# Performance work log

Measured on AMD Instinct MI355X. Metric: run time of the kernel, lower is better.

Reference implementation:

```python
import jax, jax.numpy as jnp
import numpy as np

B = 32768
STATE, BELIEF, HID, EMB, ACT = 100, 200, 200, 1024, 32
MIN_STD = 0.1

def _dense_init(key, fan_in, fan_out):
    k1, k2 = jax.random.split(key)
    scale = 1.0 / np.sqrt(fan_in)
    W = jax.random.uniform(k1, (fan_in, fan_out), jnp.float32, -scale, scale)
    b = jnp.zeros((fan_out,), jnp.float32)
    return W, b

def setup_inputs() -> dict:
    key = jax.random.key(0)
    ks = jax.random.split(key, 20)
    inp = {
        'prev_state': jax.random.normal(ks[0], (1, B, STATE), jnp.float32),
        'prev_action': jax.random.normal(ks[1], (1, B, ACT), jnp.float32),
        'prev_belief': jax.random.normal(ks[2], (1, B, BELIEF), jnp.float32),
        'observation': jax.random.normal(ks[3], (1, B, EMB), jnp.float32),
        'nonterminals': jnp.ones((1, B, 1), jnp.float32),
    }
    # fc_embed_state_action: (state+action) -> belief_dim, relu
    inp['W_sa'], inp['b_sa'] = _dense_init(ks[4], STATE + ACT, BELIEF)
    # GRUCell: carry = hidden (belief_dim), inputs = prev_belief (belief_dim)
    inp['W_ir'], inp['b_ir'] = _dense_init(ks[5], BELIEF, BELIEF)
    inp['W_iz'], inp['b_iz'] = _dense_init(ks[6], BELIEF, BELIEF)
    inp['W_in'], inp['b_in'] = _dense_init(ks[7], BELIEF, BELIEF)
    inp['W_hr'], _ = _dense_init(ks[8], BELIEF, BELIEF)   # no bias (flax GRUCell)
    inp['W_hz'], _ = _dense_init(ks[9], BELIEF, BELIEF)   # no bias
    inp['W_hn'], inp['b_hn'] = _dense_init(ks[10], BELIEF, BELIEF)
    # prior head
    inp['W_bp'], inp['b_bp'] = _dense_init(ks[11], BELIEF, HID)
    inp['W_sp'], inp['b_sp'] = _dense_init(ks[12], HID, 2 * STATE)
    # posterior head
    inp['W_bq'], inp['b_bq'] = _dense_init(ks[13], BELIEF + EMB, HID)
    inp['W_sq'], inp['b_sq'] = _dense_init(ks[14], HID, 2 * STATE)
    return inp

def reference(prev_state, prev_action, prev_belief, observation, nonterminals,
              W_sa, b_sa, W_ir, b_ir, W_iz, b_iz, W_in, b_in,
              W_hr, W_hz, W_hn, b_hn,
              W_bp, b_bp, W_sp, b_sp, W_bq, b_bq, W_sq, b_sq):
    noise_key = jax.random.key(42)  # stands in for the module's fixed self.rng
    s = prev_state * nonterminals  # broadcast mask over last dim
    # fc_embed_state_action (relu, activate_final=True)
    h = jax.nn.relu(jnp.concatenate([s, prev_action], axis=-1) @ W_sa + b_sa)
    # flax GRUCell with carry = h, inputs = prev_belief
    x = prev_belief
    r = jax.nn.sigmoid(x @ W_ir + b_ir + h @ W_hr)
    z = jax.nn.sigmoid(x @ W_iz + b_iz + h @ W_hz)
    n = jnp.tanh(x @ W_in + b_in + r * (h @ W_hn + b_hn))
    new_belief = (1.0 - z) * n + z * h
    # prior
    hp = jax.nn.relu(new_belief @ W_bp + b_bp)
    prior_out = jax.nn.relu(hp @ W_sp + b_sp)  # activate_final=True
    prior_mean, prior_std_raw = jnp.split(prior_out, 2, axis=-1)
    prior_std = jax.nn.softplus(prior_std_raw) + MIN_STD
    eps = jax.random.normal(noise_key, prior_mean.shape, prior_mean.dtype)
    prior_state = prior_mean + prior_std * eps
    # posterior
    hq = jax.nn.relu(jnp.concatenate([new_belief, observation], axis=-1) @ W_bq + b_bq)
    post_out = jax.nn.relu(hq @ W_sq + b_sq)
    post_mean, post_std_raw = jnp.split(post_out, 2, axis=-1)
    post_std = jax.nn.softplus(post_std_raw) + MIN_STD
    eps2 = jax.random.normal(noise_key, post_mean.shape, post_mean.dtype)  # same rng reused, as in source
    post_state = post_mean + post_std * eps2
    return (new_belief, prior_state, prior_mean, prior_std, post_state, post_mean, post_std)
```

## Files before the change

### kernel.cpp

```cpp
#include <hip/hip_runtime.h>
#include <stdint.h>

typedef short short8 __attribute__((ext_vector_type(8)));
typedef float floatx4 __attribute__((ext_vector_type(4)));
typedef unsigned short ushort_t;

#define BATCH 32768
#define STR   232
#define SLAB  (16*STR)
#define TOT_TILES 1391

#define M_SA 0
#define M_IR 1
#define M_HR 2
#define M_IZ 3
#define M_HZ 4
#define M_IN 5
#define M_HN 6
#define M_BP 7
#define M_SP 8
#define M_SQ 9
#define M_BQ 10

__device__ constexpr int TILE0[11] = {0,65,156,247,338,429,520,611,702,793,884};
__device__ constexpr int KLIM[11]  = {132,200,200,200,200,200,200,200,200,200,0};

__device__ __forceinline__ ushort_t f2bf(float f){
  uint32_t u = __float_as_uint(f);
  uint32_t r = (u + 0x7fffu + ((u >> 16) & 1u)) >> 16;
  return (ushort_t)r;
}
__device__ __forceinline__ float bf2f(ushort_t h){ return __uint_as_float(((uint32_t)h) << 16); }

__device__ __forceinline__ float sigmf_(float x){ return 1.f / (1.f + expf(-x)); }
__device__ __forceinline__ float softplusf_(float x){
  return fmaxf(x, 0.f) + log1pf(expf(-fabsf(x)));
}
__device__ __forceinline__ uint32_t rotl32(uint32_t x, int r){ return (x << r) | (x >> (32 - r)); }

__device__ __forceinline__ void threefry2x32_k42(uint32_t x0, uint32_t x1,
                                                 uint32_t& o0, uint32_t& o1){
  const uint32_t k0 = 0u, k1 = 42u, k2 = 0u ^ 42u ^ 0x1BD11BDAu;
  x0 += k0; x1 += k1;
#define TF_R(rot) { x0 += x1; x1 = rotl32(x1, rot); x1 ^= x0; }
  TF_R(13) TF_R(15) TF_R(26) TF_R(6)  x0 += k1; x1 += k2 + 1u;
  TF_R(17) TF_R(29) TF_R(16) TF_R(24) x0 += k2; x1 += k0 + 2u;
  TF_R(13) TF_R(15) TF_R(26) TF_R(6)  x0 += k0; x1 += k1 + 3u;
  TF_R(17) TF_R(29) TF_R(16) TF_R(24) x0 += k1; x1 += k2 + 4u;
  TF_R(13) TF_R(15) TF_R(26) TF_R(6)  x0 += k2; x1 += k0 + 5u;
#undef TF_R
  o0 = x0; o1 = x1;
}

__device__ __forceinline__ float jax_erfinv(float x){
  float w = -log1pf(-x * x);
  float p;
  if (w < 5.0f) {
    w -= 2.5f;
    p = 2.81022636e-08f;
    p = fmaf(p, w, 3.43273939e-07f);
    p = fmaf(p, w, -3.5233877e-06f);
    p = fmaf(p, w, -4.39150654e-06f);
    p = fmaf(p, w, 0.00021858087f);
    p = fmaf(p, w, -0.00125372503f);
    p = fmaf(p, w, -0.00417768164f);
    p = fmaf(p, w, 0.246640727f);
    p = fmaf(p, w, 1.50140941f);
  } else {
    w = sqrtf(w) - 3.0f;
    p = -0.000200214257f;
    p = fmaf(p, w, 0.000100950558f);
    p = fmaf(p, w, 0.00134934322f);
    p = fmaf(p, w, -0.00367342844f);
    p = fmaf(p, w, 0.00573950773f);
    p = fmaf(p, w, -0.0076224613f);
    p = fmaf(p, w, 0.00943887047f);
    p = fmaf(p, w, 1.00167406f);
    p = fmaf(p, w, 2.83297682f);
  }
  return p * x;
}

__device__ __forceinline__ float jax_normal_at(uint32_t j){
  uint32_t o0, o1;
  threefry2x32_k42(0u, j, o0, o1);
  uint32_t bits = o0 ^ o1;
  const float lo = -0.99999994f;
  float f = __uint_as_float((bits >> 9) | 0x3f800000u) - 1.0f;
  float fm = f * 1.99999994f;
  float u = fmaxf(lo, fm + lo);
  return 1.41421356f * jax_erfinv(u);
}

struct ConvP { const float* src[11]; ushort_t* dst; };

__global__ void __launch_bounds__(64) convw(ConvP cp)
{
  int t = blockIdx.x;
  int lane = threadIdx.x;
  const int cum[12] = {0,65,156,247,338,429,520,611,702,793,884,1391};
  int mi = 0;
  #pragma unroll
  for (int i = 0; i < 11; ++i) if (t >= cum[i+1]) mi = i+1;
  int lt = t - cum[mi];
  int kb = lt / 13, nt = lt - kb*13;
  const float* S = cp.src[mi];
  int q = lane >> 4, m = lane & 15;
  int n = nt*16 + m;
  ushort_t* D = cp.dst + (size_t)t*512 + lane*8;
  #pragma unroll
  for (int j = 0; j < 8; ++j){
    int k = kb*32 + q*8 + j;
    float v = 0.f;
    if (n < 200){
      if (mi == 10){
        if (k < 200) v = S[k*200+n];
        else if (k >= 224) v = S[(size_t)(k-24)*200+n];
      } else {
        int K = (mi == 0) ? 132 : 200;
        if (k < K) v = S[k*200+n];
      }
    }
    D[j] = f2bf(v);
  }
}

struct MainP {
  const float* prev_state; const float* prev_action; const float* prev_belief;
  const float* observation; const float* nonterm;
  const float* b_sa; const float* b_ir; const float* b_iz; const float* b_in; const float* b_hn;
  const float* b_bp; const float* b_sp; const float* b_bq; const float* b_sq;
  const float* W[11];
  const ushort_t* ws;
  float* out;
};

__device__ __forceinline__ short8 afrag(const ushort_t* buf, int m, int kb, int q){
  return *(const short8*)(buf + m*STR + kb*32 + q*8);
}

#define NSTEPS 214
#define STAGE_US 3584

struct Sched {
  short t0[NSTEPS]; signed char cnt[NSTEPS];
  constexpr Sched() : t0(), cnt() {
    int s = 0;
    for (int kb = 0; kb < 5; ++kb){
      t0[s] = (short)(0 + kb*13);     cnt[s] = 7; ++s;
      t0[s] = (short)(0 + kb*13 + 7); cnt[s] = 6; ++s;
    }
    for (int kb = 0; kb < 7; ++kb)
      for (int mt = 1; mt <= 6; ++mt){ t0[s] = (short)(65 + 91*(mt-1) + kb*13);     cnt[s] = 7; ++s; }
    for (int kb = 0; kb < 7; ++kb)
      for (int mt = 1; mt <= 6; ++mt){ t0[s] = (short)(65 + 91*(mt-1) + kb*13 + 7); cnt[s] = 6; ++s; }
    for (int kb = 0; kb < 7; ++kb){
      t0[s] = (short)(611 + kb*13);     cnt[s] = 7; ++s;
      t0[s] = (short)(611 + kb*13 + 7); cnt[s] = 6; ++s;
    }
    for (int kb = 0; kb < 7; ++kb){
      t0[s] = (short)(702 + kb*13);     cnt[s] = 7; ++s;
      t0[s] = (short)(702 + kb*13 + 7); cnt[s] = 6; ++s;
    }
    for (int kb = 0; kb < 39; ++kb){
      t0[s] = (short)(884 + kb*13);     cnt[s] = 7; ++s;
      t0[s] = (short)(884 + kb*13 + 7); cnt[s] = 6; ++s;
    }
    for (int kb = 0; kb < 7; ++kb){
      t0[s] = (short)(793 + kb*13);     cnt[s] = 7; ++s;
      t0[s] = (short)(793 + kb*13 + 7); cnt[s] = 6; ++s;
    }
  }
};
__device__ constexpr Sched SCHED{};

__device__ __forceinline__ void stage_issue(const ushort_t* ws, ushort_t* sbuf,
                                            int step, int w, int lane)
{
  if (step >= NSTEPS) return;
  const int t0 = SCHED.t0[step];
  const int cn = SCHED.cnt[step];
  ushort_t* dstb = sbuf + (step % 3) * STAGE_US;
  const ushort_t* srcb = ws + ((size_t)t0 << 9) + (lane << 3);
  #pragma unroll
  for (int r = 0; r < 2; ++r){
    int tt = w + r*4;
    if (tt < cn){
      __builtin_amdgcn_global_load_lds(
        (const __attribute__((address_space(1))) uint32_t*)(const void*)(srcb + (tt << 9)),
        (__attribute__((address_space(3)))       uint32_t*)(void*)(dstb + (tt << 9)),
        16, 0, 0);
    }
  }
}

__device__ __forceinline__ short8 sfrag(const ushort_t* sbuf, int step, int j, int lane){
  return *(const short8*)(sbuf + (step % 3) * STAGE_US + (j << 9) + (lane << 3));
}

__device__ __forceinline__ void step_sync(int sidx, int w, int extra)
{
  int n2 = 0;
  if (sidx + 2 < NSTEPS){
    int cn = SCHED.cnt[sidx + 2];
    n2 = (w < cn ? 1 : 0) + ((w + 4) < cn ? 1 : 0);
  }
  int nw = n2 + extra;
  switch (nw){
    case 0:  asm volatile("s_waitcnt vmcnt(0)" ::: "memory"); break;
    case 1:  asm volatile("s_waitcnt vmcnt(1)" ::: "memory"); break;
    case 2:  asm volatile("s_waitcnt vmcnt(2)" ::: "memory"); break;
    case 3:  asm volatile("s_waitcnt vmcnt(3)" ::: "memory"); break;
    default: asm volatile("s_waitcnt vmcnt(4)" ::: "memory"); break;
  }
  __builtin_amdgcn_s_barrier();
}

__device__ __forceinline__ void gemm13_kb(const MainP& p, ushort_t* stageb, int& sidx,
    const ushort_t* asrc, floatx4 (&acc)[13], int kb, int m, int q, int lane, int w)
{
  short8 a = afrag(asrc, m, kb, q);
  stage_issue(p.ws, stageb, sidx+2, w, lane);
  #pragma unroll
  for (int j = 0; j < 7; ++j)
    acc[j] = __builtin_amdgcn_mfma_f32_16x16x32_bf16(a, sfrag(stageb, sidx, j, lane), acc[j], 0,0,0);
  step_sync(sidx, w, 0); ++sidx;
  stage_issue(p.ws, stageb, sidx+2, w, lane);
  #pragma unroll
  for (int j = 0; j < 6; ++j)
    acc[7+j] = __builtin_amdgcn_mfma_f32_16x16x32_bf16(a, sfrag(stageb, sidx, j, lane), acc[7+j], 0,0,0);
  step_sync(sidx, w, 0); ++sidx;
}

template<int CNT, int NT0>
__device__ __forceinline__ void gru_chunk_staged(const MainP& p, ushort_t* stageb, int& sidx,
    const ushort_t* bufX, const ushort_t* bufH, int R0, int m, int q, int lane, int w,
    floatx4 (&nbv)[13])
{
  floatx4 aR[CNT], aZ[CNT], aXN[CNT], aHN[CNT];
  #pragma unroll
  for (int i = 0; i < CNT; ++i){
    int col = (NT0+i)*16 + m;
    float br = (col<200)? p.b_ir[col] : 0.f;
    float bz = (col<200)? p.b_iz[col] : 0.f;
    float bn = (col<200)? p.b_in[col] : 0.f;
    float bh = (col<200)? p.b_hn[col] : 0.f;
    aR[i]  = (floatx4){br,br,br,br};
    aZ[i]  = (floatx4){bz,bz,bz,bz};
    aXN[i] = (floatx4){bn,bn,bn,bn};
    aHN[i] = (floatx4){bh,bh,bh,bh};
  }
#define GRU_STEP(AV, ACC) \
  stage_issue(p.ws, stageb, sidx+2, w, lane); \
  _Pragma("unroll") \
  for (int i = 0; i < CNT; ++i) \
    ACC[i] = __builtin_amdgcn_mfma_f32_16x16x32_bf16(AV, sfrag(stageb, sidx, i, lane), ACC[i], 0,0,0); \
  step_sync(sidx, w, 0); ++sidx;

  #pragma unroll 1
  for (int kb = 0; kb < 7; ++kb){
    short8 ax = afrag(bufX, m, kb, q);
    short8 ah = afrag(bufH, m, kb, q);
    GRU_STEP(ax, aR)
    GRU_STEP(ah, aR)
    GRU_STEP(ax, aZ)
    GRU_STEP(ah, aZ)
    GRU_STEP(ax, aXN)
    GRU_STEP(ah, aHN)
  }
#undef GRU_STEP
  #pragma unroll
  for (int i = 0; i < CNT; ++i){
    int col = (NT0+i)*16 + m;
    if (col < 200){
      #pragma unroll
      for (int rg = 0; rg < 4; ++rg){
        int rowl = q*4 + rg;
        float rr = sigmf_(aR[i][rg]);
        float zz = sigmf_(aZ[i][rg]);
        float nn = tanhf(fmaf(rr, aHN[i][rg], aXN[i][rg]));
        float hv = bf2f(bufH[rowl*STR + col]);
        float nb = fmaf(zz, hv - nn, nn);
        nbv[NT0+i][rg] = nb;
        __builtin_nontemporal_store(nb, &p.out[(size_t)(R0+rowl)*200 + col]);
      }
    }
  }
}

__device__ __forceinline__ void head_out(const floatx4* acc, float* sdb,
    float* o_state, float* o_mean, float* o_std, int R0, int m, int q)
{
  #pragma unroll
  for (int nt = 6; nt < 13; ++nt){
    int col = nt*16 + m;
    if (col >= 100 && col < 200){
      #pragma unroll
      for (int rg = 0; rg < 4; ++rg){
        int rowl = q*4 + rg;
        float sr = fmaxf(acc[nt][rg], 0.f);
        float sd = softplusf_(sr) + 0.1f;
        sdb[rowl*100 + (col-100)] = sd;
        __builtin_nontemporal_store(sd, &o_std[(size_t)(R0+rowl)*100 + (col-100)]);
      }
    }
  }
  #pragma unroll
  for (int nt = 0; nt < 7; ++nt){
    int col = nt*16 + m;
    if (col < 100){
      #pragma unroll
      for (int rg = 0; rg < 4; ++rg){
        int rowl = q*4 + rg;
        float mean = fmaxf(acc[nt][rg], 0.f);
        float sd = sdb[rowl*100 + col];
        float e = jax_normal_at((uint32_t)(R0+rowl)*100u + (uint32_t)col);
        __builtin_nontemporal_store(mean, &o_mean[(size_t)(R0+rowl)*100 + col]);
        __builtin_nontemporal_store(fmaf(sd, e, mean), &o_state[(size_t)(R0+rowl)*100 + col]);
      }
    }
  }
}

__global__ void __launch_bounds__(256, 2) rssm_staged(MainP p)
{
  __shared__ __align__(16) ushort_t lds[8*SLAB + 3*STAGE_US];

  const int tid  = threadIdx.x;
  const int w    = tid >> 6;
  const int lane = tid & 63;
  const int q    = lane >> 4;
  const int m    = lane & 15;
  const int R0   = blockIdx.x * 64 + w * 16;

  ushort_t* bufX   = lds + w * 2 * SLAB;
  ushort_t* bufH   = bufX + SLAB;
  ushort_t* stageb = lds + 8*SLAB;
  int sidx = 0;

  stage_issue(p.ws, stageb, 0, w, lane);
  stage_issue(p.ws, stageb, 1, w, lane);

  for (int t = lane; t < 16*160; t += 64){
    int rr = t / 160, cc = t - rr*160;
    int grow = R0 + rr;
    float v = 0.f;
    if (cc < 100)      v = p.prev_state[(size_t)grow*100 + cc] * p.nonterm[grow];
    else if (cc < 132) v = p.prev_action[(size_t)grow*32 + (cc-100)];
    bufX[rr*STR + cc] = f2bf(v);
  }
  for (int t = lane; t < 16*24; t += 64){
    int rr = t / 24, cc = 200 + (t - rr*24);
    bufH[rr*STR + cc] = 0;
  }
  asm volatile("s_waitcnt vmcnt(0)" ::: "memory");
  __builtin_amdgcn_s_barrier();

  {
    floatx4 acc[13];
    #pragma unroll
    for (int nt = 0; nt < 13; ++nt){
      int col = nt*16 + m;
      float bv = (col<200)? p.b_sa[col] : 0.f;
      acc[nt] = (floatx4){bv,bv,bv,bv};
    }
    #pragma unroll 1
    for (int kb = 0; kb < 5; ++kb)
      gemm13_kb(p, stageb, sidx, bufX, acc, kb, m, q, lane, w);
    #pragma unroll
    for (int nt = 0; nt < 13; ++nt){
      int col = nt*16 + m;
      if (col < 200){
        #pragma unroll
        for (int rg = 0; rg < 4; ++rg)
          bufH[(q*4+rg)*STR + col] = f2bf(fmaxf(acc[nt][rg], 0.f));
      }
    }
  }

  for (int t = lane; t < 16*224; t += 64){
    int rr = t / 224, cc = t - rr*224;
    float v = 0.f;
    if (cc < 200)
      v = __builtin_nontemporal_load(&p.prev_belief[(size_t)(R0+rr)*200 + cc]);
    bufX[rr*STR + cc] = f2bf(v);
  }

  floatx4 nbv[13];
  gru_chunk_staged<7,0>(p, stageb, sidx, bufX, bufH, R0, m, q, lane, w, nbv);
  gru_chunk_staged<6,7>(p, stageb, sidx, bufX, bufH, R0, m, q, lane, w, nbv);

  #pragma unroll
  for (int nt = 0; nt < 13; ++nt){
    int col = nt*16 + m;
    if (col < 200){
      #pragma unroll
      for (int rg = 0; rg < 4; ++rg)
        bufX[(q*4+rg)*STR + col] = f2bf(nbv[nt][rg]);
    }
  }

  {
    floatx4 acc[13];
    #pragma unroll
    for (int nt = 0; nt < 13; ++nt){
      int col = nt*16 + m;
      float bv = (col<200)? p.b_bp[col] : 0.f;
      acc[nt] = (floatx4){bv,bv,bv,bv};
    }
    #pragma unroll 1
    for (int kb = 0; kb < 7; ++kb)
      gemm13_kb(p, stageb, sidx, bufX, acc, kb, m, q, lane, w);
    #pragma unroll
    for (int nt = 0; nt < 13; ++nt){
      int col = nt*16 + m;
      if (col < 200){
        #pragma unroll
        for (int rg = 0; rg < 4; ++rg)
          bufH[(q*4+rg)*STR + col] = f2bf(fmaxf(acc[nt][rg], 0.f));
      }
    }
  }

  {
    floatx4 acc[13];
    #pragma unroll
    for (int nt = 0; nt < 13; ++nt){
      int col = nt*16 + m;
      float bv = (col<200)? p.b_sp[col] : 0.f;
      acc[nt] = (floatx4){bv,bv,bv,bv};
    }
    #pragma unroll 1
    for (int kb = 0; kb < 7; ++kb)
      gemm13_kb(p, stageb, sidx, bufH, acc, kb, m, q, lane, w);
    head_out(acc, (float*)bufH,
             p.out + (size_t)BATCH*200, p.out + (size_t)BATCH*300, p.out + (size_t)BATCH*400,
             R0, m, q);
  }

  {
    floatx4 acc[13];
    #pragma unroll
    for (int nt = 0; nt < 13; ++nt){
      int col = nt*16 + m;
      float bv = (col<200)? p.b_bq[col] : 0.f;
      acc[nt] = (floatx4){bv,bv,bv,bv};
    }
    #pragma unroll 1
    for (int kb = 0; kb < 7; ++kb)
      gemm13_kb(p, stageb, sidx, bufX, acc, kb, m, q, lane, w);

    const float* orow_base = p.observation + (size_t)(R0+m)*1024;
    floatx4 o1 = __builtin_nontemporal_load((const floatx4*)(orow_base + q*8));
    floatx4 o2 = __builtin_nontemporal_load((const floatx4*)(orow_base + q*8 + 4));
    #pragma unroll 1
    for (int kb = 7; kb < 39; ++kb){
      short8 ao;
      ao[0] = (short)f2bf(o1[0]); ao[1] = (short)f2bf(o1[1]);
      ao[2] = (short)f2bf(o1[2]); ao[3] = (short)f2bf(o1[3]);
      ao[4] = (short)f2bf(o2[0]); ao[5] = (short)f2bf(o2[1]);
      ao[6] = (short)f2bf(o2[2]); ao[7] = (short)f2bf(o2[3]);
      stage_issue(p.ws, stageb, sidx+2, w, lane);
      #pragma unroll
      for (int j = 0; j < 7; ++j)
        acc[j] = __builtin_amdgcn_mfma_f32_16x16x32_bf16(ao, sfrag(stageb, sidx, j, lane), acc[j], 0,0,0);
      step_sync(sidx, w, 0); ++sidx;
      floatx4 nn1 = {0,0,0,0}, nn2 = {0,0,0,0};
      int ex = 0;
      if (kb < 38){
        const float* nr = orow_base + ((kb+1)*32 - 224) + q*8;
        nn1 = __builtin_nontemporal_load((const floatx4*)(nr));
        nn2 = __builtin_nontemporal_load((const floatx4*)(nr + 4));
        ex = 2;
      }
      __builtin_amdgcn_sched_barrier(0);
      stage_issue(p.ws, stageb, sidx+2, w, lane);
      #pragma unroll
      for (int j = 0; j < 6; ++j)
        acc[7+j] = __builtin_amdgcn_mfma_f32_16x16x32_bf16(ao, sfrag(stageb, sidx, j, lane), acc[7+j], 0,0,0);
      step_sync(sidx, w, ex); ++sidx;
      o1 = nn1; o2 = nn2;
    }
    #pragma unroll
    for (int nt = 0; nt < 13; ++nt){
      int col = nt*16 + m;
      if (col < 200){
        #pragma unroll
        for (int rg = 0; rg < 4; ++rg)
          bufH[(q*4+rg)*STR + col] = f2bf(fmaxf(acc[nt][rg], 0.f));
      }
    }
    for (int t = lane; t < 16*24; t += 64){
      int rr = t / 24, cc = 200 + (t - rr*24);
      bufH[rr*STR + cc] = 0;
    }
  }

  {
    floatx4 acc[13];
    #pragma unroll
    for (int nt = 0; nt < 13; ++nt){
      int col = nt*16 + m;
      float bv = (col<200)? p.b_sq[col] : 0.f;
      acc[nt] = (floatx4){bv,bv,bv,bv};
    }
    #pragma unroll 1
    for (int kb = 0; kb < 7; ++kb)
      gemm13_kb(p, stageb, sidx, bufH, acc, kb, m, q, lane, w);
    head_out(acc, (float*)bufX,
             p.out + (size_t)BATCH*500, p.out + (size_t)BATCH*600, p.out + (size_t)BATCH*700,
             R0, m, q);
  }
}

template<int MAT>
__device__ __forceinline__ short8 bfr0(const MainP& p, int kb, int nt, int lane, int q, int m){
  int n = nt*16 + m;
  const float* S = p.W[MAT];
  uint32_t u[8];
  #pragma unroll
  for (int j = 0; j < 8; ++j){
    int k = kb*32 + q*8 + j;
    int srow;
    if (MAT == M_BQ) srow = (k < 200) ? k : ((k >= 224) ? k - 24 : -1);
    else             srow = (k < KLIM[MAT]) ? k : -1;
    float v = (srow >= 0 && n < 200) ? S[(size_t)srow*200 + n] : 0.f;
    u[j] = __float_as_uint(v);
  }
  short8 r;
  #pragma unroll
  for (int j = 0; j < 8; ++j) r[j] = (short)(u[j] >> 16);
  return r;
}

template<int CNT, int NT0>
__device__ __forceinline__ void gru_chunk0(const MainP& p,
    const ushort_t* bufX, const ushort_t* bufH, int R0, int m, int q, int lane,
    floatx4 (&nbv)[13])
{
  floatx4 aR[CNT], aZ[CNT], aXN[CNT], aHN[CNT];
  #pragma unroll
  for (int i = 0; i < CNT; ++i){
    int col = (NT0+i)*16 + m;
    float br = (col<200)? p.b_ir[col] : 0.f;
    float bz = (col<200)? p.b_iz[col] : 0.f;
    float bn = (col<200)? p.b_in[col] : 0.f;
    float bh = (col<200)? p.b_hn[col] : 0.f;
    aR[i]  = (floatx4){br,br,br,br};
    aZ[i]  = (floatx4){bz,bz,bz,bz};
    aXN[i] = (floatx4){bn,bn,bn,bn};
    aHN[i] = (floatx4){bh,bh,bh,bh};
  }
  #pragma unroll 1
  for (int kb = 0; kb < 7; ++kb){
    short8 ax = afrag(bufX, m, kb, q);
    short8 ah = afrag(bufH, m, kb, q);
    #pragma unroll
    for (int i = 0; i < CNT; ++i){
      int nt = NT0 + i;
      aR[i]  = __builtin_amdgcn_mfma_f32_16x16x32_bf16(ax, bfr0<M_IR>(p,kb,nt,lane,q,m), aR[i], 0,0,0);
      aR[i]  = __builtin_amdgcn_mfma_f32_16x16x32_bf16(ah, bfr0<M_HR>(p,kb,nt,lane,q,m), aR[i], 0,0,0);
      aZ[i]  = __builtin_amdgcn_mfma_f32_16x16x32_bf16(ax, bfr0<M_IZ>(p,kb,nt,lane,q,m), aZ[i], 0,0,0);
      aZ[i]  = __builtin_amdgcn_mfma_f32_16x16x32_bf16(ah, bfr0<M_HZ>(p,kb,nt,lane,q,m), aZ[i], 0,0,0);
      aXN[i] = __builtin_amdgcn_mfma_f32_16x16x32_bf16(ax, bfr0<M_IN>(p,kb,nt,lane,q,m), aXN[i], 0,0,0);
      aHN[i] = __builtin_amdgcn_mfma_f32_16x16x32_bf16(ah, bfr0<M_HN>(p,kb,nt,lane,q,m), aHN[i], 0,0,0);
    }
  }
  #pragma unroll
  for (int i = 0; i < CNT; ++i){
    int col = (NT0+i)*16 + m;
    if (col < 200){
      #pragma unroll
      for (int rg = 0; rg < 4; ++rg){
        int rowl = q*4 + rg;
        float rr = sigmf_(aR[i][rg]);
        float zz = sigmf_(aZ[i][rg]);
        float nn = tanhf(fmaf(rr, aHN[i][rg], aXN[i][rg]));
        float hv = bf2f(bufH[rowl*STR + col]);
        float nb = fmaf(zz, hv - nn, nn);
        nbv[NT0+i][rg] = nb;
        __builtin_nontemporal_store(nb, &p.out[(size_t)(R0+rowl)*200 + col]);
      }
    }
  }
}

__global__ void __launch_bounds__(256, 2) rssm_direct(MainP p)
{
  __shared__ __align__(16) ushort_t lds[4 * 2 * SLAB];

  const int tid  = threadIdx.x;
  const int w    = tid >> 6;
  const int lane = tid & 63;
  const int q    = lane >> 4;
  const int m    = lane & 15;
  const int R0   = blockIdx.x * 64 + w * 16;

  ushort_t* bufX = lds + w * 2 * SLAB;
  ushort_t* bufH = bufX + SLAB;

  for (int t = lane; t < 16*160; t += 64){
    int rr = t / 160, cc = t - rr*160;
    int grow = R0 + rr;
    float v = 0.f;
    if (cc < 100)      v = p.prev_state[(size_t)grow*100 + cc] * p.nonterm[grow];
    else if (cc < 132) v = p.prev_action[(size_t)grow*32 + (cc-100)];
    bufX[rr*STR + cc] = f2bf(v);
  }
  for (int t = lane; t < 16*24; t += 64){
    int rr = t / 24, cc = 200 + (t - rr*24);
    bufH[rr*STR + cc] = 0;
  }
  __syncthreads();

  {
    floatx4 acc[13];
    #pragma unroll
    for (int nt = 0; nt < 13; ++nt){
      int col = nt*16 + m;
      float bv = (col<200)? p.b_sa[col] : 0.f;
      acc[nt] = (floatx4){bv,bv,bv,bv};
    }
    #pragma unroll 1
    for (int kb = 0; kb < 5; ++kb){
      short8 a = afrag(bufX, m, kb, q);
      #pragma unroll
      for (int nt = 0; nt < 13; ++nt)
        acc[nt] = __builtin_amdgcn_mfma_f32_16x16x32_bf16(a, bfr0<M_SA>(p,kb,nt,lane,q,m), acc[nt], 0,0,0);
    }
    #pragma unroll
    for (int nt = 0; nt < 13; ++nt){
      int col = nt*16 + m;
      if (col < 200){
        #pragma unroll
        for (int rg = 0; rg < 4; ++rg)
          bufH[(q*4+rg)*STR + col] = f2bf(fmaxf(acc[nt][rg], 0.f));
      }
    }
  }

  for (int t = lane; t < 16*224; t += 64){
    int rr = t / 224, cc = t - rr*224;
    float v = 0.f;
    if (cc < 200)
      v = __builtin_nontemporal_load(&p.prev_belief[(size_t)(R0+rr)*200 + cc]);
    bufX[rr*STR + cc] = f2bf(v);
  }
  __syncthreads();

  floatx4 nbv[13];
  gru_chunk0<7,0>(p, bufX, bufH, R0, m, q, lane, nbv);
  gru_chunk0<6,7>(p, bufX, bufH, R0, m, q, lane, nbv);

  #pragma unroll
  for (int nt = 0; nt < 13; ++nt){
    int col = nt*16 + m;
    if (col < 200){
      #pragma unroll
      for (int rg = 0; rg < 4; ++rg)
        bufX[(q*4+rg)*STR + col] = f2bf(nbv[nt][rg]);
    }
  }

  {
    floatx4 acc[13];
    #pragma unroll
    for (int nt = 0; nt < 13; ++nt){
      int col = nt*16 + m;
      float bv = (col<200)? p.b_bp[col] : 0.f;
      acc[nt] = (floatx4){bv,bv,bv,bv};
    }
    #pragma unroll 1
    for (int kb = 0; kb < 7; ++kb){
      short8 a = afrag(bufX, m, kb, q);
      #pragma unroll
      for (int nt = 0; nt < 13; ++nt)
        acc[nt] = __builtin_amdgcn_mfma_f32_16x16x32_bf16(a, bfr0<M_BP>(p,kb,nt,lane,q,m), acc[nt], 0,0,0);
    }
    #pragma unroll
    for (int nt = 0; nt < 13; ++nt){
      int col = nt*16 + m;
      if (col < 200){
        #pragma unroll
        for (int rg = 0; rg < 4; ++rg)
          bufH[(q*4+rg)*STR + col] = f2bf(fmaxf(acc[nt][rg], 0.f));
      }
    }
  }
  __syncthreads();

  {
    floatx4 acc[13];
    #pragma unroll
    for (int nt = 0; nt < 13; ++nt){
      int col = nt*16 + m;
      float bv = (col<200)? p.b_sp[col] : 0.f;
      acc[nt] = (floatx4){bv,bv,bv,bv};
    }
    #pragma unroll 1
    for (int kb = 0; kb < 7; ++kb){
      short8 a = afrag(bufH, m, kb, q);
      #pragma unroll
      for (int nt = 0; nt < 13; ++nt)
        acc[nt] = __builtin_amdgcn_mfma_f32_16x16x32_bf16(a, bfr0<M_SP>(p,kb,nt,lane,q,m), acc[nt], 0,0,0);
    }
    head_out(acc, (float*)bufH,
             p.out + (size_t)BATCH*200, p.out + (size_t)BATCH*300, p.out + (size_t)BATCH*400,
             R0, m, q);
  }
  __syncthreads();

  {
    floatx4 acc[13];
    #pragma unroll
    for (int nt = 0; nt < 13; ++nt){
      int col = nt*16 + m;
      float bv = (col<200)? p.b_bq[col] : 0.f;
      acc[nt] = (floatx4){bv,bv,bv,bv};
    }
    #pragma unroll 1
    for (int kb = 0; kb < 7; ++kb){
      short8 a = afrag(bufX, m, kb, q);
      #pragma unroll
      for (int nt = 0; nt < 13; ++nt)
        acc[nt] = __builtin_amdgcn_mfma_f32_16x16x32_bf16(a, bfr0<M_BQ>(p,kb,nt,lane,q,m), acc[nt], 0,0,0);
    }
    const float* orow_base = p.observation + (size_t)(R0+m)*1024;
    #pragma unroll 1
    for (int kb = 7; kb < 39; ++kb){
      const float* orow = orow_base + (kb*32 - 224) + q*8;
      floatx4 o1 = __builtin_nontemporal_load((const floatx4*)(orow));
      floatx4 o2 = __builtin_nontemporal_load((const floatx4*)(orow + 4));
      short8 ao;
      ao[0] = (short)f2bf(o1[0]); ao[1] = (short)f2bf(o1[1]);
      ao[2] = (short)f2bf(o1[2]); ao[3] = (short)f2bf(o1[3]);
      ao[4] = (short)f2bf(o2[0]); ao[5] = (short)f2bf(o2[1]);
      ao[6] = (short)f2bf(o2[2]); ao[7] = (short)f2bf(o2[3]);
      #pragma unroll
      for (int nt = 0; nt < 13; ++nt)
        acc[nt] = __builtin_amdgcn_mfma_f32_16x16x32_bf16(ao, bfr0<M_BQ>(p,kb,nt,lane,q,m), acc[nt], 0,0,0);
    }
    #pragma unroll
    for (int nt = 0; nt < 13; ++nt){
      int col = nt*16 + m;
      if (col < 200){
        #pragma unroll
        for (int rg = 0; rg < 4; ++rg)
          bufH[(q*4+rg)*STR + col] = f2bf(fmaxf(acc[nt][rg], 0.f));
      }
    }
    for (int t = lane; t < 16*24; t += 64){
      int rr = t / 24, cc = 200 + (t - rr*24);
      bufH[rr*STR + cc] = 0;
    }
  }
  __syncthreads();

  {
    floatx4 acc[13];
    #pragma unroll
    for (int nt = 0; nt < 13; ++nt){
      int col = nt*16 + m;
      float bv = (col<200)? p.b_sq[col] : 0.f;
      acc[nt] = (floatx4){bv,bv,bv,bv};
    }
    #pragma unroll 1
    for (int kb = 0; kb < 7; ++kb){
      short8 a = afrag(bufH, m, kb, q);
      #pragma unroll
      for (int nt = 0; nt < 13; ++nt)
        acc[nt] = __builtin_amdgcn_mfma_f32_16x16x32_bf16(a, bfr0<M_SQ>(p,kb,nt,lane,q,m), acc[nt], 0,0,0);
    }
    head_out(acc, (float*)bufX,
             p.out + (size_t)BATCH*500, p.out + (size_t)BATCH*600, p.out + (size_t)BATCH*700,
             R0, m, q);
  }
}

extern "C" void kernel_launch(void* const* d_in, const int* in_sizes, int n_in,
                              void* d_out, int out_size, void* d_ws, size_t ws_size,
                              hipStream_t stream)
{
  MainP p;
  p.prev_state  = (const float*)d_in[0];
  p.prev_action = (const float*)d_in[1];
  p.prev_belief = (const float*)d_in[2];
  p.observation = (const float*)d_in[3];
  p.nonterm     = (const float*)d_in[4];
  p.b_sa = (const float*)d_in[6];
  p.b_ir = (const float*)d_in[8];
  p.b_iz = (const float*)d_in[10];
  p.b_in = (const float*)d_in[12];
  p.b_hn = (const float*)d_in[16];
  p.b_bp = (const float*)d_in[18];
  p.b_sp = (const float*)d_in[20];
  p.b_bq = (const float*)d_in[22];
  p.b_sq = (const float*)d_in[24];
  p.W[M_SA] = (const float*)d_in[5];
  p.W[M_IR] = (const float*)d_in[7];
  p.W[M_HR] = (const float*)d_in[13];
  p.W[M_IZ] = (const float*)d_in[9];
  p.W[M_HZ] = (const float*)d_in[14];
  p.W[M_IN] = (const float*)d_in[11];
  p.W[M_HN] = (const float*)d_in[15];
  p.W[M_BP] = (const float*)d_in[17];
  p.W[M_SP] = (const float*)d_in[19];
  p.W[M_SQ] = (const float*)d_in[23];
  p.W[M_BQ] = (const float*)d_in[21];
  p.ws   = (const ushort_t*)d_ws;
  p.out  = (float*)d_out;

  bool use_ws = (ws_size >= (size_t)TOT_TILES * 1024u);
  if (use_ws){
    ConvP cp;
    cp.src[0]  = p.W[M_SA]; cp.src[1]  = p.W[M_IR]; cp.src[2]  = p.W[M_HR];
    cp.src[3]  = p.W[M_IZ]; cp.src[4]  = p.W[M_HZ]; cp.src[5]  = p.W[M_IN];
    cp.src[6]  = p.W[M_HN]; cp.src[7]  = p.W[M_BP]; cp.src[8]  = p.W[M_SP];
    cp.src[9]  = p.W[M_SQ]; cp.src[10] = p.W[M_BQ];
    cp.dst     = (ushort_t*)d_ws;
    convw<<<TOT_TILES, 64, 0, stream>>>(cp);
    rssm_staged<<<512, 256, 0, stream>>>(p);
  } else {
    rssm_direct<<<512, 256, 0, stream>>>(p);
  }
}
```

Baseline: 513.9 us.

## Process 32 rows per wave to reuse each staged weight fragment twice

The staged kernel now gives each wave two 16-row groups (32 rows) instead of one. Every B fragment loaded from the LDS staging ring therefore feeds two MFMAs. Blocks shrink from 4 waves to 2, so each wave issues up to 4 global-to-LDS loads per step and the vmcnt waits are extended to match. The goal is to halve the LDS weight reads and barrier steps per row. The cost is doubled accumulator register pressure and fewer waves per block to hide latency.

```diff
diff --git a/kernel.cpp b/kernel.cpp
--- a/kernel.cpp
+++ b/kernel.cpp
@@ -7,6 +7,8 @@
 
 #define BATCH 32768
 #define STR   232
+#define RW    32
+#define SLAB2 (RW*STR)
 #define SLAB  (16*STR)
 #define TOT_TILES 1391
 
@@ -135,6 +137,9 @@
   float* out;
 };
 
+__device__ __forceinline__ short8 afrag_g(const ushort_t* buf, int g, int m, int kb, int q){
+  return *(const short8*)(buf + (g*16 + m)*STR + kb*32 + q*8);
+}
 __device__ __forceinline__ short8 afrag(const ushort_t* buf, int m, int kb, int q){
   return *(const short8*)(buf + m*STR + kb*32 + q*8);
 }
@@ -183,8 +188,8 @@
   ushort_t* dstb = sbuf + (step % 3) * STAGE_US;
   const ushort_t* srcb = ws + ((size_t)t0 << 9) + (lane << 3);
   #pragma unroll
-  for (int r = 0; r < 2; ++r){
-    int tt = w + r*4;
+  for (int r = 0; r < 4; ++r){
+    int tt = w + r*2;
     if (tt < cn){
       __builtin_amdgcn_global_load_lds(
         (const __attribute__((address_space(1))) uint32_t*)(const void*)(srcb + (tt << 9)),
@@ -203,7 +208,7 @@
   int n2 = 0;
   if (sidx + 2 < NSTEPS){
     int cn = SCHED.cnt[sidx + 2];
-    n2 = (w < cn ? 1 : 0) + ((w + 4) < cn ? 1 : 0);
+    n2 = (w < cn) ? ((cn - w + 1) >> 1) : 0;
   }
   int nw = n2 + extra;
   switch (nw){
@@ -211,30 +216,422 @@
     case 1:  asm volatile("s_waitcnt vmcnt(1)" ::: "memory"); break;
     case 2:  asm volatile("s_waitcnt vmcnt(2)" ::: "memory"); break;
     case 3:  asm volatile("s_waitcnt vmcnt(3)" ::: "memory"); break;
-    default: asm volatile("s_waitcnt vmcnt(4)" ::: "memory"); break;
+    case 4:  asm volatile("s_waitcnt vmcnt(4)" ::: "memory"); break;
+    case 5:  asm volatile("s_waitcnt vmcnt(5)" ::: "memory"); break;
+    case 6:  asm volatile("s_waitcnt vmcnt(6)" ::: "memory"); break;
+    case 7:  asm volatile("s_waitcnt vmcnt(7)" ::: "memory"); break;
+    default: asm volatile("s_waitcnt vmcnt(8)" ::: "memory"); break;
   }
   __builtin_amdgcn_s_barrier();
 }
 
 __device__ __forceinline__ void gemm13_kb(const MainP& p, ushort_t* stageb, int& sidx,
-    const ushort_t* asrc, floatx4 (&acc)[13], int kb, int m, int q, int lane, int w)
-{
-  short8 a = afrag(asrc, m, kb, q);
+    const ushort_t* asrc, floatx4 (&acc)[2][13], int kb, int m, int q, int lane, int w)
+{
+  short8 a0 = afrag_g(asrc, 0, m, kb, q);
+  short8 a1 = afrag_g(asrc, 1, m, kb, q);
   stage_issue(p.ws, stageb, sidx+2, w, lane);
   #pragma unroll
-  for (int j = 0; j < 7; ++j)
-    acc[j] = __builtin_amdgcn_mfma_f32_16x16x32_bf16(a, sfrag(stageb, sidx, j, lane), acc[j], 0,0,0);
+  for (int j = 0; j < 7; ++j){
+    short8 b = sfrag(stageb, sidx, j, lane);
+    acc[0][j] = __builtin_amdgcn_mfma_f32_16x16x32_bf16(a0, b, acc[0][j], 0,0,0);
+    acc[1][j] = __builtin_amdgcn_mfma_f32_16x16x32_bf16(a1, b, acc[1][j], 0,0,0);
+  }
   step_sync(sidx, w, 0); ++sidx;
   stage_issue(p.ws, stageb, sidx+2, w, lane);
   #pragma unroll
-  for (int j = 0; j < 6; ++j)
-    acc[7+j] = __builtin_amdgcn_mfma_f32_16x16x32_bf16(a, sfrag(stageb, sidx, j, lane), acc[7+j], 0,0,0);
+  for (int j = 0; j < 6; ++j){
+    short8 b = sfrag(stageb, sidx, j, lane);
+    acc[0][7+j] = __builtin_amdgcn_mfma_f32_16x16x32_bf16(a0, b, acc[0][7+j], 0,0,0);
+    acc[1][7+j] = __builtin_amdgcn_mfma_f32_16x16x32_bf16(a1, b, acc[1][7+j], 0,0,0);
+  }
   step_sync(sidx, w, 0); ++sidx;
 }
 
 template<int CNT, int NT0>
 __device__ __forceinline__ void gru_chunk_staged(const MainP& p, ushort_t* stageb, int& sidx,
     const ushort_t* bufX, const ushort_t* bufH, int R0, int m, int q, int lane, int w,
+    floatx4 (&nbv)[2][13])
+{
+  floatx4 aR[2][CNT], aZ[2][CNT], aXN[2][CNT], aHN[2][CNT];
+  #pragma unroll
+  for (int i = 0; i < CNT; ++i){
+    int col = (NT0+i)*16 + m;
+    float br = (col<200)? p.b_ir[col] : 0.f;
+    float bz = (col<200)? p.b_iz[col] : 0.f;
+    float bn = (col<200)? p.b_in[col] : 0.f;
+    float bh = (col<200)? p.b_hn[col] : 0.f;
+    #pragma unroll
+    for (int g = 0; g < 2; ++g){
+      aR[g][i]  = (floatx4){br,br,br,br};
+      aZ[g][i]  = (floatx4){bz,bz,bz,bz};
+      aXN[g][i] = (floatx4){bn,bn,bn,bn};
+      aHN[g][i] = (floatx4){bh,bh,bh,bh};
+    }
+  }
+#define GRU_STEP(AV0, AV1, ACC) \
+  stage_issue(p.ws, stageb, sidx+2, w, lane); \
+  _Pragma("unroll") \
+  for (int i = 0; i < CNT; ++i){ \
+    short8 b_ = sfrag(stageb, sidx, i, lane); \
+    ACC[0][i] = __builtin_amdgcn_mfma_f32_16x16x32_bf16(AV0, b_, ACC[0][i], 0,0,0); \
+    ACC[1][i] = __builtin_amdgcn_mfma_f32_16x16x32_bf16(AV1, b_, ACC[1][i], 0,0,0); \
+  } \
+  step_sync(sidx, w, 0); ++sidx;
+
+  #pragma unroll 1
+  for (int kb = 0; kb < 7; ++kb){
+    short8 ax0 = afrag_g(bufX, 0, m, kb, q);
+    short8 ax1 = afrag_g(bufX, 1, m, kb, q);
+    short8 ah0 = afrag_g(bufH, 0, m, kb, q);
+    short8 ah1 = afrag_g(bufH, 1, m, kb, q);
+    GRU_STEP(ax0, ax1, aR)
+    GRU_STEP(ah0, ah1, aR)
+    GRU_STEP(ax0, ax1, aZ)
+    GRU_STEP(ah0, ah1, aZ)
+    GRU_STEP(ax0, ax1, aXN)
+    GRU_STEP(ah0, ah1, aHN)
+  }
+#undef GRU_STEP
+  #pragma unroll
+  for (int g = 0; g < 2; ++g){
+    #pragma unroll
+    for (int i = 0; i < CNT; ++i){
+      int col = (NT0+i)*16 + m;
+      if (col < 200){
+        #pragma unroll
+        for (int rg = 0; rg < 4; ++rg){
+          int rowl = g*16 + q*4 + rg;
+          float rr = sigmf_(aR[g][i][rg]);
+          float zz = sigmf_(aZ[g][i][rg]);
+          float nn = tanhf(fmaf(rr, aHN[g][i][rg], aXN[g][i][rg]));
+          float hv = bf2f(bufH[rowl*STR + col]);
+          float nb = fmaf(zz, hv - nn, nn);
+          nbv[g][NT0+i][rg] = nb;
+          __builtin_nontemporal_store(nb, &p.out[(size_t)(R0+rowl)*200 + col]);
+        }
+      }
+    }
+  }
+}
+
+__device__ __forceinline__ void head_out(const floatx4 (&acc)[2][13], float* sdb,
+    float* o_state, float* o_mean, float* o_std, int R0, int m, int q)
+{
+  #pragma unroll
+  for (int nt = 6; nt < 13; ++nt){
+    int col = nt*16 + m;
+    if (col >= 100 && col < 200){
+      #pragma unroll
+      for (int g = 0; g < 2; ++g){
+        #pragma unroll
+        for (int rg = 0; rg < 4; ++rg){
+          int rowl = g*16 + q*4 + rg;
+          float sr = fmaxf(acc[g][nt][rg], 0.f);
+          float sd = softplusf_(sr) + 0.1f;
+          sdb[rowl*100 + (col-100)] = sd;
+          __builtin_nontemporal_store(sd, &o_std[(size_t)(R0+rowl)*100 + (col-100)]);
+        }
+      }
+    }
+  }
+  #pragma unroll
+  for (int nt = 0; nt < 7; ++nt){
+    int col = nt*16 + m;
+    if (col < 100){
+      #pragma unroll
+      for (int g = 0; g < 2; ++g){
+        #pragma unroll
+        for (int rg = 0; rg < 4; ++rg){
+          int rowl = g*16 + q*4 + rg;
+          float mean = fmaxf(acc[g][nt][rg], 0.f);
+          float sd = sdb[rowl*100 + col];
+          float e = jax_normal_at((uint32_t)(R0+rowl)*100u + (uint32_t)col);
+          __builtin_nontemporal_store(mean, &o_mean[(size_t)(R0+rowl)*100 + col]);
+          __builtin_nontemporal_store(fmaf(sd, e, mean), &o_state[(size_t)(R0+rowl)*100 + col]);
+        }
+      }
+    }
+  }
+}
+
+__global__ void __launch_bounds__(128, 1) rssm_staged(MainP p)
+{
+  __shared__ __align__(16) ushort_t lds[4*SLAB2 + 3*STAGE_US];
+
+  const int tid  = threadIdx.x;
+  const int w    = tid >> 6;
+  const int lane = tid & 63;
+  const int q    = lane >> 4;
+  const int m    = lane & 15;
+  const int R0   = blockIdx.x * 64 + w * RW;
+
+  ushort_t* bufX   = lds + w * 2 * SLAB2;
+  ushort_t* bufH   = bufX + SLAB2;
+  ushort_t* stageb = lds + 4*SLAB2;
+  int sidx = 0;
+
+  stage_issue(p.ws, stageb, 0, w, lane);
+  stage_issue(p.ws, stageb, 1, w, lane);
+
+  for (int t = lane; t < RW*160; t += 64){
+    int rr = t / 160, cc = t - rr*160;
+    int grow = R0 + rr;
+    float v = 0.f;
+    if (cc < 100)      v = p.prev_state[(size_t)grow*100 + cc] * p.nonterm[grow];
+    else if (cc < 132) v = p.prev_action[(size_t)grow*32 + (cc-100)];
+    bufX[rr*STR + cc] = f2bf(v);
+  }
+  for (int t = lane; t < RW*24; t += 64){
+    int rr = t / 24, cc = 200 + (t - rr*24);
+    bufH[rr*STR + cc] = 0;
+  }
+  asm volatile("s_waitcnt vmcnt(0)" ::: "memory");
+  __builtin_amdgcn_s_barrier();
+
+  {
+    floatx4 acc[2][13];
+    #pragma unroll
+    for (int nt = 0; nt < 13; ++nt){
+      int col = nt*16 + m;
+      float bv = (col<200)? p.b_sa[col] : 0.f;
+      acc[0][nt] = (floatx4){bv,bv,bv,bv};
+      acc[1][nt] = (floatx4){bv,bv,bv,bv};
+    }
+    #pragma unroll 1
+    for (int kb = 0; kb < 5; ++kb)
+      gemm13_kb(p, stageb, sidx, bufX, acc, kb, m, q, lane, w);
+    #pragma unroll
+    for (int g = 0; g < 2; ++g)
+      #pragma unroll
+      for (int nt = 0; nt < 13; ++nt){
+        int col = nt*16 + m;
+        if (col < 200){
+          #pragma unroll
+          for (int rg = 0; rg < 4; ++rg)
+            bufH[(g*16 + q*4+rg)*STR + col] = f2bf(fmaxf(acc[g][nt][rg], 0.f));
+        }
+      }
+  }
+
+  for (int t = lane; t < RW*224; t += 64){
+    int rr = t / 224, cc = t - rr*224;
+    float v = 0.f;
+    if (cc < 200)
+      v = __builtin_nontemporal_load(&p.prev_belief[(size_t)(R0+rr)*200 + cc]);
+    bufX[rr*STR + cc] = f2bf(v);
+  }
+
+  floatx4 nbv[2][13];
+  gru_chunk_staged<7,0>(p, stageb, sidx, bufX, bufH, R0, m, q, lane, w, nbv);
+  gru_chunk_staged<6,7>(p, stageb, sidx, bufX, bufH, R0, m, q, lane, w, nbv);
+
+  #pragma unroll
+  for (int g = 0; g < 2; ++g)
+    #pragma unroll
+    for (int nt = 0; nt < 13; ++nt){
+      int col = nt*16 + m;
+      if (col < 200){
+        #pragma unroll
+        for (int rg = 0; rg < 4; ++rg)
+          bufX[(g*16 + q*4+rg)*STR + col] = f2bf(nbv[g][nt][rg]);
+      }
+    }
+
+  {
+    floatx4 acc[2][13];
+    #pragma unroll
+    for (int nt = 0; nt < 13; ++nt){
+      int col = nt*16 + m;
+      float bv = (col<200)? p.b_bp[col] : 0.f;
+      acc[0][nt] = (floatx4){bv,bv,bv,bv};
+      acc[1][nt] = (floatx4){bv,bv,bv,bv};
+    }
+    #pragma unroll 1
+    for (int kb = 0; kb < 7; ++kb)
+      gemm13_kb(p, stageb, sidx, bufX, acc, kb, m, q, lane, w);
+    #pragma unroll
+    for (int g = 0; g < 2; ++g)
+      #pragma unroll
+      for (int nt = 0; nt < 13; ++nt){
+        int col = nt*16 + m;
+        if (col < 200){
+          #pragma unroll
+          for (int rg = 0; rg < 4; ++rg)
+            bufH[(g*16 + q*4+rg)*STR + col] = f2bf(fmaxf(acc[g][nt][rg], 0.f));
+        }
+      }
+  }
+
+  {
+    floatx4 acc[2][13];
+    #pragma unroll
+    for (int nt = 0; nt < 13; ++nt){
+      int col = nt*16 + m;
+      float bv = (col<200)? p.b_sp[col] : 0.f;
+      acc[0][nt] = (floatx4){bv,bv,bv,bv};
+      acc[1][nt] = (floatx4){bv,bv,bv,bv};
+    }
+    #pragma unroll 1
+    for (int kb = 0; kb < 7; ++kb)
+      gemm13_kb(p, stageb, sidx, bufH, acc, kb, m, q, lane, w);
+    head_out(acc, (float*)bufH,
+             p.out + (size_t)BATCH*200, p.out + (size_t)BATCH*300, p.out + (size_t)BATCH*400,
+             R0, m, q);
+  }
+
+  {
+    floatx4 acc[2][13];
+    #pragma unroll
+    for (int nt = 0; nt < 13; ++nt){
+      int col = nt*16 + m;
+      float bv = (col<200)? p.b_bq[col] : 0.f;
+      acc[0][nt] = (floatx4){bv,bv,bv,bv};
+      acc[1][nt] = (floatx4){bv,bv,bv,bv};
+    }
+    #pragma unroll 1
+    for (int kb = 0; kb < 7; ++kb)
+      gemm13_kb(p, stageb, sidx, bufX, acc, kb, m, q, lane, w);
+
+    const float* ob0 = p.observation + (size_t)(R0 + m)*1024;
+    const float* ob1 = p.observation + (size_t)(R0 + 16 + m)*1024;
+    floatx4 o00 = __builtin_nontemporal_load((const floatx4*)(ob0 + q*8));
+    floatx4 o01 = __builtin_nontemporal_load((const floatx4*)(ob0 + q*8 + 4));
+    floatx4 o10 = __builtin_nontemporal_load((const floatx4*)(ob1 + q*8));
+    floatx4 o11 = __builtin_nontemporal_load((const floatx4*)(ob1 + q*8 + 4));
+    #pragma unroll 1
+    for (int kb = 7; kb < 39; ++kb){
+      short8 ao0, ao1;
+      ao0[0] = (short)f2bf(o00[0]); ao0[1] = (short)f2bf(o00[1]);
+      ao0[2] = (short)f2bf(o00[2]); ao0[3] = (short)f2bf(o00[3]);
+      ao0[4] = (short)f2bf(o01[0]); ao0[5] = (short)f2bf(o01[1]);
+      ao0[6] = (short)f2bf(o01[2]); ao0[7] = (short)f2bf(o01[3]);
+      ao1[0] = (short)f2bf(o10[0]); ao1[1] = (short)f2bf(o10[1]);
+      ao1[2] = (short)f2bf(o10[2]); ao1[3] = (short)f2bf(o10[3]);
+      ao1[4] = (short)f2bf(o11[0]); ao1[5] = (short)f2bf(o11[1]);
+      ao1[6] = (short)f2bf(o11[2]); ao1[7] = (short)f2bf(o11[3]);
+      stage_issue(p.ws, stageb, sidx+2, w, lane);
+      #pragma unroll
+      for (int j = 0; j < 7; ++j){
+        short8 b = sfrag(stageb, sidx, j, lane);
+        acc[0][j] = __builtin_amdgcn_mfma_f32_16x16x32_bf16(ao0, b, acc[0][j], 0,0,0);
+        acc[1][j] = __builtin_amdgcn_mfma_f32_16x16x32_bf16(ao1, b, acc[1][j], 0,0,0);
+      }
+      step_sync(sidx, w, 0); ++sidx;
+      floatx4 p00 = {0,0,0,0}, p01 = {0,0,0,0}, p10 = {0,0,0,0}, p11 = {0,0,0,0};
+      int ex = 0;
+      if (kb < 38){
+        const float* nr0 = ob0 + ((kb+1)*32 - 224) + q*8;
+        const float* nr1 = ob1 + ((kb+1)*32 - 224) + q*8;
+        p00 = __builtin_nontemporal_load((const floatx4*)(nr0));
+        p01 = __builtin_nontemporal_load((const floatx4*)(nr0 + 4));
+        p10 = __builtin_nontemporal_load((const floatx4*)(nr1));
+        p11 = __builtin_nontemporal_load((const floatx4*)(nr1 + 4));
+        ex = 4;
+      }
+      __builtin_amdgcn_sched_barrier(0);
+      stage_issue(p.ws, stageb, sidx+2, w, lane);
+      #pragma unroll
+      for (int j = 0; j < 6; ++j){
+        short8 b = sfrag(stageb, sidx, j, lane);
+        acc[0][7+j] = __builtin_amdgcn_mfma_f32_16x16x32_bf16(ao0, b, acc[0][7+j], 0,0,0);
+        acc[1][7+j] = __builtin_amdgcn_mfma_f32_16x16x32_bf16(ao1, b, acc[1][7+j], 0,0,0);
+      }
+      step_sync(sidx, w, ex); ++sidx;
+      o00 = p00; o01 = p01; o10 = p10; o11 = p11;
+    }
+    #pragma unroll
+    for (int g = 0; g < 2; ++g)
+      #pragma unroll
+      for (int nt = 0; nt < 13; ++nt){
+        int col = nt*16 + m;
+        if (col < 200){
+          #pragma unroll
+          for (int rg = 0; rg < 4; ++rg)
+            bufH[(g*16 + q*4+rg)*STR + col] = f2bf(fmaxf(acc[g][nt][rg], 0.f));
+        }
+      }
+    for (int t = lane; t < RW*24; t += 64){
+      int rr = t / 24, cc = 200 + (t - rr*24);
+      bufH[rr*STR + cc] = 0;
+    }
+  }
+
+  {
+    floatx4 acc[2][13];
+    #pragma unroll
+    for (int nt = 0; nt < 13; ++nt){
+      int col = nt*16 + m;
+      float bv = (col<200)? p.b_sq[col] : 0.f;
+      acc[0][nt] = (floatx4){bv,bv,bv,bv};
+      acc[1][nt] = (floatx4){bv,bv,bv,bv};
+    }
+    #pragma unroll 1
+    for (int kb = 0; kb < 7; ++kb)
+      gemm13_kb(p, stageb, sidx, bufH, acc, kb, m, q, lane, w);
+    head_out(acc, (float*)bufX,
+             p.out + (size_t)BATCH*500, p.out + (size_t)BATCH*600, p.out + (size_t)BATCH*700,
+             R0, m, q);
+  }
+}
+
+template<int MAT>
+__device__ __forceinline__ short8 bfr0(const MainP& p, int kb, int nt, int lane, int q, int m){
+  int n = nt*16 + m;
+  const float* S = p.W[MAT];
+  uint32_t u[8];
+  #pragma unroll
+  for (int j = 0; j < 8; ++j){
+    int k = kb*32 + q*8 + j;
+    int srow;
+    if (MAT == M_BQ) srow = (k < 200) ? k : ((k >= 224) ? k - 24 : -1);
+    else             srow = (k < KLIM[MAT]) ? k : -1;
+    float v = (srow >= 0 && n < 200) ? S[(size_t)srow*200 + n] : 0.f;
+    u[j] = __float_as_uint(v);
+  }
+  short8 r;
+  #pragma unroll
+  for (int j = 0; j < 8; ++j) r[j] = (short)(u[j] >> 16);
+  return r;
+}
+
+__device__ __forceinline__ void head_out16(const floatx4* acc, float* sdb,
+    float* o_state, float* o_mean, float* o_std, int R0, int m, int q)
+{
+  #pragma unroll
+  for (int nt = 6; nt < 13; ++nt){
+    int col = nt*16 + m;
+    if (col >= 100 && col < 200){
+      #pragma unroll
+      for (int rg = 0; rg < 4; ++rg){
+        int rowl = q*4 + rg;
+        float sr = fmaxf(acc[nt][rg], 0.f);
+        float sd = softplusf_(sr) + 0.1f;
+        sdb[rowl*100 + (col-100)] = sd;
+        __builtin_nontemporal_store(sd, &o_std[(size_t)(R0+rowl)*100 + (col-100)]);
+      }
+    }
+  }
+  #pragma unroll
+  for (int nt = 0; nt < 7; ++nt){
+    int col = nt*16 + m;
+    if (col < 100){
+      #pragma unroll
+      for (int rg = 0; rg < 4; ++rg){
+        int rowl = q*4 + rg;
+        float mean = fmaxf(acc[nt][rg], 0.f);
+        float sd = sdb[rowl*100 + col];
+        float e = jax_normal_at((uint32_t)(R0+rowl)*100u + (uint32_t)col);
+        __builtin_nontemporal_store(mean, &o_mean[(size_t)(R0+rowl)*100 + col]);
+        __builtin_nontemporal_store(fmaf(sd, e, mean), &o_state[(size_t)(R0+rowl)*100 + col]);
+      }
+    }
+  }
+}
+
+template<int CNT, int NT0>
+__device__ __forceinline__ void gru_chunk0(const MainP& p,
+    const ushort_t* bufX, const ushort_t* bufH, int R0, int m, int q, int lane,
     floatx4 (&nbv)[13])
 {
   floatx4 aR[CNT], aZ[CNT], aXN[CNT], aHN[CNT];
@@ -250,25 +647,21 @@
     aXN[i] = (floatx4){bn,bn,bn,bn};
     aHN[i] = (floatx4){bh,bh,bh,bh};
   }
-#define GRU_STEP(AV, ACC) \
-  stage_issue(p.ws, stageb, sidx+2, w, lane); \
-  _Pragma("unroll") \
-  for (int i = 0; i < CNT; ++i) \
-    ACC[i] = __builtin_amdgcn_mfma_f32_16x16x32_bf16(AV, sfrag(stageb, sidx, i, lane), ACC[i], 0,0,0); \
-  step_sync(sidx, w, 0); ++sidx;
-
   #pragma unroll 1
   for (int kb = 0; kb < 7; ++kb){
     short8 ax = afrag(bufX, m, kb, q);
     short8 ah = afrag(bufH, m, kb, q);
-    GRU_STEP(ax, aR)
-    GRU_STEP(ah, aR)
-    GRU_STEP(ax, aZ)
-    GRU_STEP(ah, aZ)
-    GRU_STEP(ax, aXN)
-    GRU_STEP(ah, aHN)
-  }
-#undef GRU_STEP
+    #pragma unroll
+    for (int i = 0; i < CNT; ++i){
+      int nt = NT0 + i;
+      aR[i]  = __builtin_amdgcn_mfma_f32_16x16x32_bf16(ax, bfr0<M_IR>(p,kb,nt,lane,q,m), aR[i], 0,0,0);
+      aR[i]  = __builtin_amdgcn_mfma_f32_16x16x32_bf16(ah, bfr0<M_HR>(p,kb,nt,lane,q,m), aR[i], 0,0,0);
+      aZ[i]  = __builtin_amdgcn_mfma_f32_16x16x32_bf16(ax, bfr0<M_IZ>(p,kb,nt,lane,q,m), aZ[i], 0,0,0);
+      aZ[i]  = __builtin_amdgcn_mfma_f32_16x16x32_bf16(ah, bfr0<M_HZ>(p,kb,nt,lane,q,m), aZ[i], 0,0,0);
+      aXN[i] = __builtin_amdgcn_mfma_f32_16x16x32_bf16(ax, bfr0<M_IN>(p,kb,nt,lane,q,m), aXN[i], 0,0,0);
+      aHN[i] = __builtin_amdgcn_mfma_f32_16x16x32_bf16(ah, bfr0<M_HN>(p,kb,nt,lane,q,m), aHN[i], 0,0,0);
+    }
+  }
   #pragma unroll
   for (int i = 0; i < CNT; ++i){
     int col = (NT0+i)*16 + m;
@@ -288,43 +681,9 @@
   }
 }
 
-__device__ __forceinline__ void head_out(const floatx4* acc, float* sdb,
-    float* o_state, float* o_mean, float* o_std, int R0, int m, int q)
-{
-  #pragma unroll
-  for (int nt = 6; nt < 13; ++nt){
-    int col = nt*16 + m;
-    if (col >= 100 && col < 200){
-      #pragma unroll
-      for (int rg = 0; rg < 4; ++rg){
-        int rowl = q*4 + rg;
-        float sr = fmaxf(acc[nt][rg], 0.f);
-        float sd = softplusf_(sr) + 0.1f;
-        sdb[rowl*100 + (col-100)] = sd;
-        __builtin_nontemporal_store(sd, &o_std[(size_t)(R0+rowl)*100 + (col-100)]);
-      }
-    }
-  }
-  #pragma unroll
-  for (int nt = 0; nt < 7; ++nt){
-    int col = nt*16 + m;
-    if (col < 100){
-      #pragma unroll
-      for (int rg = 0; rg < 4; ++rg){
-        int rowl = q*4 + rg;
-        float mean = fmaxf(acc[nt][rg], 0.f);
-        float sd = sdb[rowl*100 + col];
-        float e = jax_normal_at((uint32_t)(R0+rowl)*100u + (uint32_t)col);
-        __builtin_nontemporal_store(mean, &o_mean[(size_t)(R0+rowl)*100 + col]);
-        __builtin_nontemporal_store(fmaf(sd, e, mean), &o_state[(size_t)(R0+rowl)*100 + col]);
-      }
-    }
-  }
-}
-
-__global__ void __launch_bounds__(256, 2) rssm_staged(MainP p)
-{
-  __shared__ __align__(16) ushort_t lds[8*SLAB + 3*STAGE_US];
+__global__ void __launch_bounds__(256, 2) rssm_direct(MainP p)
+{
+  __shared__ __align__(16) ushort_t lds[4 * 2 * SLAB];
 
   const int tid  = threadIdx.x;
   const int w    = tid >> 6;
@@ -333,13 +692,8 @@
   const int m    = lane & 15;
   const int R0   = blockIdx.x * 64 + w * 16;
 
-  ushort_t* bufX   = lds + w * 2 * SLAB;
-  ushort_t* bufH   = bufX + SLAB;
-  ushort_t* stageb = lds + 8*SLAB;
-  int sidx = 0;
-
-  stage_issue(p.ws, stageb, 0, w, lane);
-  stage_issue(p.ws, stageb, 1, w, lane);
+  ushort_t* bufX = lds + w * 2 * SLAB;
+  ushort_t* bufH = bufX + SLAB;
 
   for (int t = lane; t < 16*160; t += 64){
     int rr = t / 160, cc = t - rr*160;
@@ -353,8 +707,7 @@
     int rr = t / 24, cc = 200 + (t - rr*24);
     bufH[rr*STR + cc] = 0;
   }
-  asm volatile("s_waitcnt vmcnt(0)" ::: "memory");
-  __builtin_amdgcn_s_barrier();
+  __syncthreads();
 
   {
     floatx4 acc[13];
@@ -365,8 +718,12 @@
       acc[nt] = (floatx4){bv,bv,bv,bv};
     }
     #pragma unroll 1
-    for (int kb = 0; kb < 5; ++kb)
-      gemm13_kb(p, stageb, sidx, bufX, acc, kb, m, q, lane, w);
+    for (int kb = 0; kb < 5; ++kb){
+      short8 a = afrag(bufX, m, kb, q);
+      #pragma unroll
+      for (int nt = 0; nt < 13; ++nt)
+        acc[nt] = __builtin_amdgcn_mfma_f32_16x16x32_bf16(a, bfr0<M_SA>(p,kb,nt,lane,q,m), acc[nt], 0,0,0);
+    }
     #pragma unroll
     for (int nt = 0; nt < 13; ++nt){
       int col = nt*16 + m;
@@ -385,10 +742,11 @@
       v = __builtin_nontemporal_load(&p.prev_belief[(size_t)(R0+rr)*200 + cc]);
     bufX[rr*STR + cc] = f2bf(v);
   }
+  __syncthreads();
 
   floatx4 nbv[13];
-  gru_chunk_staged<7,0>(p, stageb, sidx, bufX, bufH, R0, m, q, lane, w, nbv);
-  gru_chunk_staged<6,7>(p, stageb, sidx, bufX, bufH, R0, m, q, lane, w, nbv);
+  gru_chunk0<7,0>(p, bufX, bufH, R0, m, q, lane, nbv);
+  gru_chunk0<6,7>(p, bufX, bufH, R0, m, q, lane, nbv);
 
   #pragma unroll
   for (int nt = 0; nt < 13; ++nt){
@@ -409,8 +767,12 @@
       acc[nt] = (floatx4){bv,bv,bv,bv};
     }
     #pragma unroll 1
-    for (int kb = 0; kb < 7; ++kb)
-      gemm13_kb(p, stageb, sidx, bufX, acc, kb, m, q, lane, w);
+    for (int kb = 0; kb < 7; ++kb){
+      short8 a = afrag(bufX, m, kb, q);
+      #pragma unroll
+      for (int nt = 0; nt < 13; ++nt)
+        acc[nt] = __builtin_amdgcn_mfma_f32_16x16x32_bf16(a, bfr0<M_BP>(p,kb,nt,lane,q,m), acc[nt], 0,0,0);
+    }
     #pragma unroll
     for (int nt = 0; nt < 13; ++nt){
       int col = nt*16 + m;
@@ -421,6 +783,7 @@
       }
     }
   }
+  __syncthreads();
 
   {
     floatx4 acc[13];
@@ -431,280 +794,13 @@
       acc[nt] = (floatx4){bv,bv,bv,bv};
     }
     #pragma unroll 1
-    for (int kb = 0; kb < 7; ++kb)
-      gemm13_kb(p, stageb, sidx, bufH, acc, kb, m, q, lane, w);
-    head_out(acc, (float*)bufH,
-             p.out + (size_t)BATCH*200, p.out + (size_t)BATCH*300, p.out + (size_t)BATCH*400,
-             R0, m, q);
-  }
-
-  {
-    floatx4 acc[13];
-    #pragma unroll
-    for (int nt = 0; nt < 13; ++nt){
-      int col = nt*16 + m;
-      float bv = (col<200)? p.b_bq[col] : 0.f;
-      acc[nt] = (floatx4){bv,bv,bv,bv};
-    }
-    #pragma unroll 1
-    for (int kb = 0; kb < 7; ++kb)
-      gemm13_kb(p, stageb, sidx, bufX, acc, kb, m, q, lane, w);
-
-    const float* orow_base = p.observation + (size_t)(R0+m)*1024;
-    floatx4 o1 = __builtin_nontemporal_load((const floatx4*)(orow_base + q*8));
-    floatx4 o2 = __builtin_nontemporal_load((const floatx4*)(orow_base + q*8 + 4));
-    #pragma unroll 1
-    for (int kb = 7; kb < 39; ++kb){
-      short8 ao;
-      ao[0] = (short)f2bf(o1[0]); ao[1] = (short)f2bf(o1[1]);
-      ao[2] = (short)f2bf(o1[2]); ao[3] = (short)f2bf(o1[3]);
-      ao[4] = (short)f2bf(o2[0]); ao[5] = (short)f2bf(o2[1]);
-      ao[6] = (short)f2bf(o2[2]); ao[7] = (short)f2bf(o2[3]);
-      stage_issue(p.ws, stageb, sidx+2, w, lane);
-      #pragma unroll
-      for (int j = 0; j < 7; ++j)
-        acc[j] = __builtin_amdgcn_mfma_f32_16x16x32_bf16(ao, sfrag(stageb, sidx, j, lane), acc[j], 0,0,0);
-      step_sync(sidx, w, 0); ++sidx;
-      floatx4 nn1 = {0,0,0,0}, nn2 = {0,0,0,0};
-      int ex = 0;
-      if (kb < 38){
-        const float* nr = orow_base + ((kb+1)*32 - 224) + q*8;
-        nn1 = __builtin_nontemporal_load((const floatx4*)(nr));
-        nn2 = __builtin_nontemporal_load((const floatx4*)(nr + 4));
-        ex = 2;
-      }
-      __builtin_amdgcn_sched_barrier(0);
-      stage_issue(p.ws, stageb, sidx+2, w, lane);
-      #pragma unroll
-      for (int j = 0; j < 6; ++j)
-        acc[7+j] = __builtin_amdgcn_mfma_f32_16x16x32_bf16(ao, sfrag(stageb, sidx, j, lane), acc[7+j], 0,0,0);
-      step_sync(sidx, w, ex); ++sidx;
-      o1 = nn1; o2 = nn2;
-    }
-    #pragma unroll
-    for (int nt = 0; nt < 13; ++nt){
-      int col = nt*16 + m;
-      if (col < 200){
-        #pragma unroll
-        for (int rg = 0; rg < 4; ++rg)
-          bufH[(q*4+rg)*STR + col] = f2bf(fmaxf(acc[nt][rg], 0.f));
-      }
-    }
-    for (int t = lane; t < 16*24; t += 64){
-      int rr = t / 24, cc = 200 + (t - rr*24);
-      bufH[rr*STR + cc] = 0;
-    }
-  }
-
-  {
-    floatx4 acc[13];
-    #pragma unroll
-    for (int nt = 0; nt < 13; ++nt){
-      int col = nt*16 + m;
-      float bv = (col<200)? p.b_sq[col] : 0.f;
-      acc[nt] = (floatx4){bv,bv,bv,bv};
-    }
-    #pragma unroll 1
-    for (int kb = 0; kb < 7; ++kb)
-      gemm13_kb(p, stageb, sidx, bufH, acc, kb, m, q, lane, w);
-    head_out(acc, (float*)bufX,
-             p.out + (size_t)BATCH*500, p.out + (size_t)BATCH*600, p.out + (size_t)BATCH*700,
-             R0, m, q);
-  }
-}
-
-template<int MAT>
-__device__ __forceinline__ short8 bfr0(const MainP& p, int kb, int nt, int lane, int q, int m){
-  int n = nt*16 + m;
-  const float* S = p.W[MAT];
-  uint32_t u[8];
-  #pragma unroll
-  for (int j = 0; j < 8; ++j){
-    int k = kb*32 + q*8 + j;
-    int srow;
-    if (MAT == M_BQ) srow = (k < 200) ? k : ((k >= 224) ? k - 24 : -1);
-    else             srow = (k < KLIM[MAT]) ? k : -1;
-    float v = (srow >= 0 && n < 200) ? S[(size_t)srow*200 + n] : 0.f;
-    u[j] = __float_as_uint(v);
-  }
-  short8 r;
-  #pragma unroll
-  for (int j = 0; j < 8; ++j) r[j] = (short)(u[j] >> 16);
-  return r;
-}
-
-template<int CNT, int NT0>
-__device__ __forceinline__ void gru_chunk0(const MainP& p,
-    const ushort_t* bufX, const ushort_t* bufH, int R0, int m, int q, int lane,
-    floatx4 (&nbv)[13])
-{
-  floatx4 aR[CNT], aZ[CNT], aXN[CNT], aHN[CNT];
-  #pragma unroll
-  for (int i = 0; i < CNT; ++i){
-    int col = (NT0+i)*16 + m;
-    float br = (col<200)? p.b_ir[col] : 0.f;
-    float bz = (col<200)? p.b_iz[col] : 0.f;
-    float bn = (col<200)? p.b_in[col] : 0.f;
-    float bh = (col<200)? p.b_hn[col] : 0.f;
-    aR[i]  = (floatx4){br,br,br,br};
-    aZ[i]  = (floatx4){bz,bz,bz,bz};
-    aXN[i] = (floatx4){bn,bn,bn,bn};
-    aHN[i] = (floatx4){bh,bh,bh,bh};
-  }
-  #pragma unroll 1
-  for (int kb = 0; kb < 7; ++kb){
-    short8 ax = afrag(bufX, m, kb, q);
-    short8 ah = afrag(bufH, m, kb, q);
-    #pragma unroll
-    for (int i = 0; i < CNT; ++i){
-      int nt = NT0 + i;
-      aR[i]  = __builtin_amdgcn_mfma_f32_16x16x32_bf16(ax, bfr0<M_IR>(p,kb,nt,lane,q,m), aR[i], 0,0,0);
-      aR[i]  = __builtin_amdgcn_mfma_f32_16x16x32_bf16(ah, bfr0<M_HR>(p,kb,nt,lane,q,m), aR[i], 0,0,0);
-      aZ[i]  = __builtin_amdgcn_mfma_f32_16x16x32_bf16(ax, bfr0<M_IZ>(p,kb,nt,lane,q,m), aZ[i], 0,0,0);
-      aZ[i]  = __builtin_amdgcn_mfma_f32_16x16x32_bf16(ah, bfr0<M_HZ>(p,kb,nt,lane,q,m), aZ[i], 0,0,0);
-      aXN[i] = __builtin_amdgcn_mfma_f32_16x16x32_bf16(ax, bfr0<M_IN>(p,kb,nt,lane,q,m), aXN[i], 0,0,0);
-      aHN[i] = __builtin_amdgcn_mfma_f32_16x16x32_bf16(ah, bfr0<M_HN>(p,kb,nt,lane,q,m), aHN[i], 0,0,0);
-    }
-  }
-  #pragma unroll
-  for (int i = 0; i < CNT; ++i){
-    int col = (NT0+i)*16 + m;
-    if (col < 200){
-      #pragma unroll
-      for (int rg = 0; rg < 4; ++rg){
-        int rowl = q*4 + rg;
-        float rr = sigmf_(aR[i][rg]);
-        float zz = sigmf_(aZ[i][rg]);
-        float nn = tanhf(fmaf(rr, aHN[i][rg], aXN[i][rg]));
-        float hv = bf2f(bufH[rowl*STR + col]);
-        float nb = fmaf(zz, hv - nn, nn);
-        nbv[NT0+i][rg] = nb;
-        __builtin_nontemporal_store(nb, &p.out[(size_t)(R0+rowl)*200 + col]);
-      }
-    }
-  }
-}
-
-__global__ void __launch_bounds__(256, 2) rssm_direct(MainP p)
-{
-  __shared__ __align__(16) ushort_t lds[4 * 2 * SLAB];
-
-  const int tid  = threadIdx.x;
-  const int w    = tid >> 6;
-  const int lane = tid & 63;
-  const int q    = lane >> 4;
-  const int m    = lane & 15;
-  const int R0   = blockIdx.x * 64 + w * 16;
-
-  ushort_t* bufX = lds + w * 2 * SLAB;
-  ushort_t* bufH = bufX + SLAB;
-
-  for (int t = lane; t < 16*160; t += 64){
-    int rr = t / 160, cc = t - rr*160;
-    int grow = R0 + rr;
-    float v = 0.f;
-    if (cc < 100)      v = p.prev_state[(size_t)grow*100 + cc] * p.nonterm[grow];
-    else if (cc < 132) v = p.prev_action[(size_t)grow*32 + (cc-100)];
-    bufX[rr*STR + cc] = f2bf(v);
-  }
-  for (int t = lane; t < 16*24; t += 64){
-    int rr = t / 24, cc = 200 + (t - rr*24);
-    bufH[rr*STR + cc] = 0;
-  }
-  __syncthreads();
-
-  {
-    floatx4 acc[13];
-    #pragma unroll
-    for (int nt = 0; nt < 13; ++nt){
-      int col = nt*16 + m;
-      float bv = (col<200)? p.b_sa[col] : 0.f;
-      acc[nt] = (floatx4){bv,bv,bv,bv};
-    }
-    #pragma unroll 1
-    for (int kb = 0; kb < 5; ++kb){
-      short8 a = afrag(bufX, m, kb, q);
-      #pragma unroll
-      for (int nt = 0; nt < 13; ++nt)
-        acc[nt] = __builtin_amdgcn_mfma_f32_16x16x32_bf16(a, bfr0<M_SA>(p,kb,nt,lane,q,m), acc[nt], 0,0,0);
-    }
-    #pragma unroll
-    for (int nt = 0; nt < 13; ++nt){
-      int col = nt*16 + m;
-      if (col < 200){
-        #pragma unroll
-        for (int rg = 0; rg < 4; ++rg)
-          bufH[(q*4+rg)*STR + col] = f2bf(fmaxf(acc[nt][rg], 0.f));
-      }
-    }
-  }
-
-  for (int t = lane; t < 16*224; t += 64){
-    int rr = t / 224, cc = t - rr*224;
-    float v = 0.f;
-    if (cc < 200)
-      v = __builtin_nontemporal_load(&p.prev_belief[(size_t)(R0+rr)*200 + cc]);
-    bufX[rr*STR + cc] = f2bf(v);
-  }
-  __syncthreads();
-
-  floatx4 nbv[13];
-  gru_chunk0<7,0>(p, bufX, bufH, R0, m, q, lane, nbv);
-  gru_chunk0<6,7>(p, bufX, bufH, R0, m, q, lane, nbv);
-
-  #pragma unroll
-  for (int nt = 0; nt < 13; ++nt){
-    int col = nt*16 + m;
-    if (col < 200){
-      #pragma unroll
-      for (int rg = 0; rg < 4; ++rg)
-        bufX[(q*4+rg)*STR + col] = f2bf(nbv[nt][rg]);
-    }
-  }
-
-  {
-    floatx4 acc[13];
-    #pragma unroll
-    for (int nt = 0; nt < 13; ++nt){
-      int col = nt*16 + m;
-      float bv = (col<200)? p.b_bp[col] : 0.f;
-      acc[nt] = (floatx4){bv,bv,bv,bv};
-    }
-    #pragma unroll 1
-    for (int kb = 0; kb < 7; ++kb){
-      short8 a = afrag(bufX, m, kb, q);
-      #pragma unroll
-      for (int nt = 0; nt < 13; ++nt)
-        acc[nt] = __builtin_amdgcn_mfma_f32_16x16x32_bf16(a, bfr0<M_BP>(p,kb,nt,lane,q,m), acc[nt], 0,0,0);
-    }
-    #pragma unroll
-    for (int nt = 0; nt < 13; ++nt){
-      int col = nt*16 + m;
-      if (col < 200){
-        #pragma unroll
-        for (int rg = 0; rg < 4; ++rg)
-          bufH[(q*4+rg)*STR + col] = f2bf(fmaxf(acc[nt][rg], 0.f));
-      }
-    }
-  }
-  __syncthreads();
-
-  {
-    floatx4 acc[13];
-    #pragma unroll
-    for (int nt = 0; nt < 13; ++nt){
-      int col = nt*16 + m;
-      float bv = (col<200)? p.b_sp[col] : 0.f;
-      acc[nt] = (floatx4){bv,bv,bv,bv};
-    }
-    #pragma unroll 1
     for (int kb = 0; kb < 7; ++kb){
       short8 a = afrag(bufH, m, kb, q);
       #pragma unroll
       for (int nt = 0; nt < 13; ++nt)
         acc[nt] = __builtin_amdgcn_mfma_f32_16x16x32_bf16(a, bfr0<M_SP>(p,kb,nt,lane,q,m), acc[nt], 0,0,0);
     }
-    head_out(acc, (float*)bufH,
+    head_out16(acc, (float*)bufH,
              p.out + (size_t)BATCH*200, p.out + (size_t)BATCH*300, p.out + (size_t)BATCH*400,
              R0, m, q);
   }
@@ -771,7 +867,7 @@
       for (int nt = 0; nt < 13; ++nt)
         acc[nt] = __builtin_amdgcn_mfma_f32_16x16x32_bf16(a, bfr0<M_SQ>(p,kb,nt,lane,q,m), acc[nt], 0,0,0);
     }
-    head_out(acc, (float*)bufX,
+    head_out16(acc, (float*)bufX,
              p.out + (size_t)BATCH*500, p.out + (size_t)BATCH*600, p.out + (size_t)BATCH*700,
              R0, m, q);
   }
@@ -819,7 +915,7 @@
     cp.src[9]  = p.W[M_SQ]; cp.src[10] = p.W[M_BQ];
     cp.dst     = (ushort_t*)d_ws;
     convw<<<TOT_TILES, 64, 0, stream>>>(cp);
-    rssm_staged<<<512, 256, 0, stream>>>(p);
+    rssm_staged<<<512, 128, 0, stream>>>(p);
   } else {
     rssm_direct<<<512, 256, 0, stream>>>(p);
   }
```

Result: slower. 644.7 us (+25.4%).
